# Kernel optimization log

Measured on AMD Instinct MI355X. Metric: run time of the kernel, lower is better.

Reference implementation:

```python
import jax, jax.numpy as jnp
import numpy as np

HEADS = 16
DIM_HEAD = 64
SCALE = DIM_HEAD ** -0.5


def setup_inputs() -> dict:
    key = jax.random.key(0)
    k1, k2, k3, k4 = jax.random.split(key, 4)
    b, n, dim = 2, 2048, 1024
    inner = HEADS * DIM_HEAD  # 1024
    return {
        "x": jax.random.normal(k1, (b, n, dim), dtype=jnp.float32),
        "x1": jax.random.normal(k2, (b, n, dim), dtype=jnp.float32),
        "W_qkv": jax.random.normal(k3, (dim, inner * 3), dtype=jnp.float32) * (dim ** -0.5),
        "W_out": jax.random.normal(k4, (inner, dim), dtype=jnp.float32) * (inner ** -0.5),
        "b_out": jnp.zeros((dim,), dtype=jnp.float32),
    }


def _split_heads(t):
    b, n, hd = t.shape
    return t.reshape(b, n, HEADS, DIM_HEAD).transpose(0, 2, 1, 3)  # b h n d


def _merge_heads(t):
    b, h, n, d = t.shape
    return t.transpose(0, 2, 1, 3).reshape(b, n, h * d)


def reference(x, x1, W_qkv, W_out, b_out):
    qkv = jnp.split(x @ W_qkv, 3, axis=-1)
    qkv1 = jnp.split(x1 @ W_qkv, 3, axis=-1)
    q, k, v = map(_split_heads, qkv)
    q1, k1, v1 = map(_split_heads, qkv1)

    # cross attention: x queries attend to x1 keys/values, and vice versa
    attn = jax.nn.softmax(jnp.einsum('bhnd,bhmd->bhnm', q, k1) * SCALE, axis=-1)
    attn1 = jax.nn.softmax(jnp.einsum('bhnd,bhmd->bhnm', q1, k) * SCALE, axis=-1)
    out = _merge_heads(jnp.einsum('bhnm,bhmd->bhnd', attn, v1))
    out1 = _merge_heads(jnp.einsum('bhnm,bhmd->bhnd', attn1, v))

    out = out @ W_out + b_out
    out1 = out1 @ W_out + b_out
    return out, out1
```

## Files before the change

kernel.cpp:

```cpp
#include <hip/hip_runtime.h>
#include <hip/hip_bf16.h>


typedef __attribute__((ext_vector_type(8))) short short8;
typedef __attribute__((ext_vector_type(4))) float f32x4;
typedef __attribute__((ext_vector_type(16))) float f32x16;

#define MFMA_BF16(a, b, c) __builtin_amdgcn_mfma_f32_16x16x32_bf16((a), (b), (c), 0, 0, 0)
#define MFMA32(a, b, c)    __builtin_amdgcn_mfma_f32_32x32x16_bf16((a), (b), (c), 0, 0, 0)

__device__ __forceinline__ ushort f2bf(float f) {
    __hip_bfloat16 h = __float2bfloat16(f);
    return *reinterpret_cast<ushort*>(&h);
}

__device__ __forceinline__ unsigned pk2(float a, float b) {
    return (unsigned)f2bf(a) | ((unsigned)f2bf(b) << 16);
}

__device__ __forceinline__ void gload_lds16(const void* g, void* l) {
    __builtin_amdgcn_global_load_lds(
        (const __attribute__((address_space(1))) void*)g,
        (__attribute__((address_space(3))) void*)l, 16, 0, 0);
}

__global__ __launch_bounds__(256) void cvt2_k(const float* __restrict__ a,
                                              const float* __restrict__ b,
                                              ushort* __restrict__ out) {
    const int idx = blockIdx.x * 256 + threadIdx.x;
    const int half = 1048576;
    const float* src = (idx < half) ? a : b;
    const int i = (idx < half ? idx : idx - half) * 4;
    float4 v = *(const float4*)(src + i);
    ushort4 o;
    o.x = f2bf(v.x); o.y = f2bf(v.y); o.z = f2bf(v.z); o.w = f2bf(v.w);
    *(ushort4*)(out + (size_t)idx * 4) = o;
}

__global__ __launch_bounds__(256) void transpose_cvt2(const float* __restrict__ wqkv,
                                                      ushort* __restrict__ wqkv_t,
                                                      const float* __restrict__ wout,
                                                      ushort* __restrict__ wout_t) {
    __shared__ ushort tile[32][33];
    int bx = blockIdx.x;
    const float* in; ushort* out; int C;
    if (bx < 96) { in = wqkv; out = wqkv_t; C = 3072; }
    else         { bx -= 96; in = wout; out = wout_t; C = 1024; }
    const int R = 1024;
    const int c0 = bx * 32, r0 = blockIdx.y * 32;
    const int tx = threadIdx.x, ty = threadIdx.y;
#pragma unroll
    for (int i = 0; i < 4; ++i)
        tile[ty * 4 + i][tx] = f2bf(in[(size_t)(r0 + ty * 4 + i) * C + c0 + tx]);
    __syncthreads();
#pragma unroll
    for (int i = 0; i < 4; ++i)
        out[(size_t)(c0 + ty * 4 + i) * R + r0 + tx] = tile[tx][ty * 4 + i];
}

__global__ __launch_bounds__(256) void qkv_gemm(const ushort* __restrict__ xb,
                                                const ushort* __restrict__ wt,
                                                ushort* __restrict__ qb,
                                                ushort* __restrict__ kb,
                                                ushort* __restrict__ vb) {
    __shared__ __align__(16) ushort As[128 * 64];
    __shared__ __align__(16) ushort Bs[128 * 64];

    const int n0 = blockIdx.x * 128;
    const int m0 = blockIdx.y * 128;
    const int t = threadIdx.x;
    const int lane = t & 63, w = t >> 6;
    const int wm = (w >> 1) * 64, wn = (w & 1) * 64;
    const int l16 = lane & 15, lq = lane >> 4;

    const int srow = lane >> 3;
    const int scol = ((lane & 7) * 16) ^ (srow << 4);

    f32x4 acc[4][4] = {};

    for (int k0 = 0; k0 < 1024; k0 += 64) {
        __syncthreads();
#pragma unroll
        for (int c = 0; c < 4; ++c) {
            const int ch = w * 4 + c;
            const int row = ch * 8 + srow;
            gload_lds16((const char*)xb + ((size_t)(m0 + row) * 1024 + k0) * 2 + scol,
                        (char*)As + ch * 1024);
            gload_lds16((const char*)wt + ((size_t)(n0 + row) * 1024 + k0) * 2 + scol,
                        (char*)Bs + ch * 1024);
        }
        __syncthreads();
#pragma unroll
        for (int kc = 0; kc < 2; ++kc) {
            short8 a[4], b[4];
#pragma unroll
            for (int i = 0; i < 4; ++i) {
                const int row = wm + i * 16 + l16;
                a[i] = *(const short8*)((const char*)As + row * 128 +
                                        ((kc * 64 + lq * 16) ^ ((row & 7) << 4)));
            }
#pragma unroll
            for (int j = 0; j < 4; ++j) {
                const int row = wn + j * 16 + l16;
                b[j] = *(const short8*)((const char*)Bs + row * 128 +
                                        ((kc * 64 + lq * 16) ^ ((row & 7) << 4)));
            }
#pragma unroll
            for (int i = 0; i < 4; ++i)
#pragma unroll
                for (int j = 0; j < 4; ++j) acc[i][j] = MFMA_BF16(a[i], b[j], acc[i][j]);
        }
    }

    const int which = (n0 >> 10);
    const float qscale = (which == 0) ? 0.125f : 1.0f;

#pragma unroll
    for (int i = 0; i < 4; ++i) {
#pragma unroll
        for (int jj = 0; jj < 4; ++jj) {
#pragma unroll
            for (int rr = 0; rr < 4; ++rr) {
                const int m = m0 + wm + i * 16 + lq * 4 + rr;
                const int nc = n0 + wn + jj * 16 + l16;
                const ushort bv = f2bf(acc[i][jj][rr] * qscale);
                const int s = m >> 12;
                const int mm = m & 4095;
                const int rem = nc & 1023;
                const int h = rem >> 6, d = rem & 63;
                const int sb = (s << 1) | (mm >> 11);
                const int pos = mm & 2047;
                const size_t bh = (size_t)(sb * 16 + h);
                if (which == 0)      qb[(bh * 2048 + pos) * 64 + d] = bv;
                else if (which == 1) kb[(bh * 2048 + pos) * 64 + d] = bv;
                else                 vb[(bh * 64 + d) * 2048 + pos] = bv;
            }
        }
    }
}

__global__ __launch_bounds__(256, 4) void attn_k(const ushort* __restrict__ qb,
                                                 const ushort* __restrict__ kb,
                                                 const ushort* __restrict__ vb,
                                                 ushort* __restrict__ ob) {
    __shared__ __align__(16) ushort Ks[2][4096];
    __shared__ __align__(16) ushort Vs[2][4096];

    const int t = threadIdx.x, lane = t & 63, w = t >> 6;
    const int l31 = lane & 31, hi = lane >> 5;

    const int lid = blockIdx.x;
    const int xcd = lid & 7, kk = lid >> 3;
    const int qt = kk & 15;
    const int g = xcd + ((kk >> 4) << 3);
    const int h = g & 15, sb = g >> 4;
    const int s = sb >> 1, bb = sb & 1;
    const int kvsb = ((1 - s) << 1) | bb;
    const int q0 = qt * 128 + w * 32;

    const ushort* qp = qb + (size_t)(sb * 16 + h) * 2048 * 64;
    const char* kp = (const char*)(kb + (size_t)(kvsb * 16 + h) * 2048 * 64);
    const char* vp = (const char*)(vb + (size_t)(kvsb * 16 + h) * 64 * 2048);

    short8 qf[4];
#pragma unroll
    for (int c = 0; c < 4; ++c)
        qf[c] = *(const short8*)(qp + (size_t)(q0 + l31) * 64 + c * 16 + hi * 8);

    f32x16 o0 = {}, o1 = {};
    float lsum = 0.f;

    const int swl = ((lane >> 3) & 7) << 4;
    auto stage = [&](int buf, int key0) {
#pragma unroll
        for (int i = 0; i < 2; ++i) {
            const int ch = w * 2 + i;
            const int off = ch * 1024 + lane * 16;
            gload_lds16(kp + (size_t)key0 * 128 + (off ^ swl),
                        (char*)&Ks[buf][0] + ch * 1024);
            const int rd = ch * 8 + (lane >> 3);
            const int cb = (lane & 7) * 16;
            gload_lds16(vp + (size_t)rd * 4096 + (size_t)key0 * 2 + (cb ^ swl),
                        (char*)&Vs[buf][0] + ch * 1024);
        }
    };

    stage(0, 0);
    __syncthreads();

    for (int tt = 0; tt < 32; ++tt) {
        const int cur = tt & 1;
        if (tt < 31) stage(cur ^ 1, (tt + 1) * 64);

        const char* Kc = (const char*)&Ks[cur][0];
        const char* Vc = (const char*)&Vs[cur][0];
        const int sw = (l31 & 7) << 4;

        f32x16 scA = {}, scB = {};
#pragma unroll
        for (int c = 0; c < 4; ++c) {
            const int off = c * 32 + hi * 16;
            short8 ka = *(const short8*)(Kc + l31 * 128 + (off ^ sw));
            short8 kb2 = *(const short8*)(Kc + (32 + l31) * 128 + (off ^ sw));
            scA = MFMA32(ka, qf[c], scA);
            scB = MFMA32(kb2, qf[c], scB);
        }

#pragma unroll
        for (int r = 0; r < 16; ++r) scA[r] = __expf(scA[r]);
#pragma unroll
        for (int r = 0; r < 16; ++r) scB[r] = __expf(scB[r]);
        {
            float sA = (((scA[0] + scA[1]) + (scA[2] + scA[3])) +
                        ((scA[4] + scA[5]) + (scA[6] + scA[7]))) +
                       (((scA[8] + scA[9]) + (scA[10] + scA[11])) +
                        ((scA[12] + scA[13]) + (scA[14] + scA[15])));
            float sB = (((scB[0] + scB[1]) + (scB[2] + scB[3])) +
                        ((scB[4] + scB[5]) + (scB[6] + scB[7]))) +
                       (((scB[8] + scB[9]) + (scB[10] + scB[11])) +
                        ((scB[12] + scB[13]) + (scB[14] + scB[15])));
            lsum += sA + sB;
        }

#define PACK_PV(P, BASE, KS)                                                     \
        {                                                                        \
            unsigned R00 = pk2(P[BASE + 0], P[BASE + 1]);                        \
            unsigned R10 = pk2(P[BASE + 2], P[BASE + 3]);                        \
            unsigned R01 = pk2(P[BASE + 4], P[BASE + 5]);                        \
            unsigned R11 = pk2(P[BASE + 6], P[BASE + 7]);                        \
            unsigned ra = (unsigned)__shfl_xor((int)(hi ? R00 : R01), 32);       \
            unsigned rb = (unsigned)__shfl_xor((int)(hi ? R10 : R11), 32);       \
            union { unsigned u[4]; short8 s8; } ap;                              \
            ap.u[0] = hi ? ra : R00;                                             \
            ap.u[1] = hi ? rb : R10;                                             \
            ap.u[2] = hi ? R01 : ra;                                             \
            ap.u[3] = hi ? R11 : rb;                                             \
            const int vo = (KS) * 32 + hi * 16;                                  \
            short8 v0 = *(const short8*)(Vc + l31 * 128 + (vo ^ sw));            \
            short8 v1 = *(const short8*)(Vc + (32 + l31) * 128 + (vo ^ sw));     \
            o0 = MFMA32(ap.s8, v0, o0);                                          \
            o1 = MFMA32(ap.s8, v1, o1);                                          \
        }
        PACK_PV(scA, 0, 0)
        PACK_PV(scA, 8, 1)
        PACK_PV(scB, 0, 2)
        PACK_PV(scB, 8, 3)
#undef PACK_PV

        __syncthreads();
    }

    const float lf = lsum + __shfl_xor(lsum, 32);
    const size_t obase = (size_t)(sb * 2048 + q0) * 1024 + h * 64 + l31;
#pragma unroll
    for (int r = 0; r < 16; ++r) {
        const int qrow = (r & 3) + 8 * (r >> 2) + 4 * hi;
        const float invl = 1.f / __shfl(lf, qrow);
        ob[obase + (size_t)qrow * 1024]      = f2bf(o0[r] * invl);
        ob[obase + (size_t)qrow * 1024 + 32] = f2bf(o1[r] * invl);
    }
}

__global__ __launch_bounds__(256) void out_gemm(const ushort* __restrict__ ob,
                                                const ushort* __restrict__ wot,
                                                const float* __restrict__ bias,
                                                float* __restrict__ out) {
    __shared__ __align__(16) ushort As[128 * 64];
    __shared__ __align__(16) ushort Bs[128 * 64];

    const int n0 = blockIdx.x * 128;
    const int m0 = blockIdx.y * 128;
    const int t = threadIdx.x;
    const int lane = t & 63, w = t >> 6;
    const int wm = (w >> 1) * 64, wn = (w & 1) * 64;
    const int l16 = lane & 15, lq = lane >> 4;

    const int srow = lane >> 3;
    const int scol = ((lane & 7) * 16) ^ (srow << 4);

    f32x4 acc[4][4] = {};

    for (int k0 = 0; k0 < 1024; k0 += 64) {
        __syncthreads();
#pragma unroll
        for (int c = 0; c < 4; ++c) {
            const int ch = w * 4 + c;
            const int row = ch * 8 + srow;
            gload_lds16((const char*)ob + ((size_t)(m0 + row) * 1024 + k0) * 2 + scol,
                        (char*)As + ch * 1024);
            gload_lds16((const char*)wot + ((size_t)(n0 + row) * 1024 + k0) * 2 + scol,
                        (char*)Bs + ch * 1024);
        }
        __syncthreads();
#pragma unroll
        for (int kc = 0; kc < 2; ++kc) {
            short8 a[4], b[4];
#pragma unroll
            for (int i = 0; i < 4; ++i) {
                const int row = wm + i * 16 + l16;
                a[i] = *(const short8*)((const char*)As + row * 128 +
                                        ((kc * 64 + lq * 16) ^ ((row & 7) << 4)));
            }
#pragma unroll
            for (int j = 0; j < 4; ++j) {
                const int row = wn + j * 16 + l16;
                b[j] = *(const short8*)((const char*)Bs + row * 128 +
                                        ((kc * 64 + lq * 16) ^ ((row & 7) << 4)));
            }
#pragma unroll
            for (int i = 0; i < 4; ++i)
#pragma unroll
                for (int j = 0; j < 4; ++j) acc[i][j] = MFMA_BF16(a[i], b[j], acc[i][j]);
        }
    }

    float biasf[4];
#pragma unroll
    for (int jj = 0; jj < 4; ++jj) biasf[jj] = bias[n0 + wn + jj * 16 + l16];

#pragma unroll
    for (int i = 0; i < 4; ++i)
#pragma unroll
        for (int jj = 0; jj < 4; ++jj)
#pragma unroll
            for (int rr = 0; rr < 4; ++rr) {
                const int m = m0 + wm + i * 16 + lq * 4 + rr;
                const int nc = n0 + wn + jj * 16 + l16;
                out[(size_t)m * 1024 + nc] = acc[i][jj][rr] + biasf[jj];
            }
}

extern "C" void kernel_launch(void* const* d_in, const int* in_sizes, int n_in,
                              void* d_out, int out_size, void* d_ws, size_t ws_size,
                              hipStream_t stream) {
    (void)out_size; (void)ws_size;
    const float *x = nullptr, *x1 = nullptr, *wqkv = nullptr, *wout = nullptr, *bias = nullptr;
    for (int i = 0; i < n_in; ++i) {
        const int sz = in_sizes[i];
        const float* p = (const float*)d_in[i];
        if (sz == 4194304)      { if (!x) x = p; else x1 = p; }
        else if (sz == 3145728) wqkv = p;
        else if (sz == 1048576) wout = p;
        else if (sz == 1024)    bias = p;
    }
    float* out = (float*)d_out;

    ushort* ws      = (ushort*)d_ws;
    ushort* wqkv_t  = ws;
    ushort* wout_t  = wqkv_t + 3072 * 1024;
    ushort* xb      = wout_t + 1024 * 1024;
    ushort* qbuf    = xb + 8388608;
    ushort* kbuf    = qbuf + 8388608;
    ushort* vbuf    = kbuf + 8388608;
    ushort* obuf    = xb;

    cvt2_k<<<8192, 256, 0, stream>>>(x, x1, xb);
    transpose_cvt2<<<dim3(128, 32), dim3(32, 8), 0, stream>>>(wqkv, wqkv_t, wout, wout_t);
    qkv_gemm<<<dim3(24, 64), 256, 0, stream>>>(xb, wqkv_t, qbuf, kbuf, vbuf);
    attn_k<<<1024, 256, 0, stream>>>(qbuf, kbuf, vbuf, obuf);
    out_gemm<<<dim3(8, 64), 256, 0, stream>>>(obuf, wout_t, bias, out);
}
```

Baseline: 307.3 us.

## Fuse prep kernels, use exp2 with folded log2e, MFMA row sums, packed bf16 cvt

Merges the input-conversion and weight-transpose kernels into a single launch, saving one kernel launch. Folds log2(e) into the Q scale so attention can use exp2 instead of exp. The softmax denominator is now computed with an extra MFMA against a ones vector instead of scalar adds and a final shuffle. Probability packing uses the hardware v_cvt_pk_bf16_f32 instruction, and s_setprio hints are added around the MFMA sections. The MFMA row sum is taken from bf16-rounded probabilities, which changes normalization numerics slightly, and it adds MFMA work to each tile.

```diff
diff --git a/kernel.cpp b/kernel.cpp
--- a/kernel.cpp
+++ b/kernel.cpp
@@ -14,8 +14,10 @@
     return *reinterpret_cast<ushort*>(&h);
 }
 
-__device__ __forceinline__ unsigned pk2(float a, float b) {
-    return (unsigned)f2bf(a) | ((unsigned)f2bf(b) << 16);
+__device__ __forceinline__ unsigned cvtpk(float lo, float hi) {
+    unsigned r;
+    asm("v_cvt_pk_bf16_f32 %0, %1, %2" : "=v"(r) : "v"(lo), "v"(hi));
+    return r;
 }
 
 __device__ __forceinline__ void gload_lds16(const void* g, void* l) {
@@ -24,31 +26,35 @@
         (__attribute__((address_space(3))) void*)l, 16, 0, 0);
 }
 
-__global__ __launch_bounds__(256) void cvt2_k(const float* __restrict__ a,
-                                              const float* __restrict__ b,
-                                              ushort* __restrict__ out) {
-    const int idx = blockIdx.x * 256 + threadIdx.x;
-    const int half = 1048576;
-    const float* src = (idx < half) ? a : b;
-    const int i = (idx < half ? idx : idx - half) * 4;
-    float4 v = *(const float4*)(src + i);
-    ushort4 o;
-    o.x = f2bf(v.x); o.y = f2bf(v.y); o.z = f2bf(v.z); o.w = f2bf(v.w);
-    *(ushort4*)(out + (size_t)idx * 4) = o;
-}
-
-__global__ __launch_bounds__(256) void transpose_cvt2(const float* __restrict__ wqkv,
-                                                      ushort* __restrict__ wqkv_t,
-                                                      const float* __restrict__ wout,
-                                                      ushort* __restrict__ wout_t) {
+__global__ __launch_bounds__(256) void prep_k(const float* __restrict__ x,
+                                              const float* __restrict__ x1,
+                                              ushort* __restrict__ xb,
+                                              const float* __restrict__ wqkv,
+                                              ushort* __restrict__ wqkv_t,
+                                              const float* __restrict__ wout,
+                                              ushort* __restrict__ wout_t) {
     __shared__ ushort tile[32][33];
-    int bx = blockIdx.x;
+    const int b = blockIdx.x;
+    if (b < 8192) {
+        const int idx = b * 256 + threadIdx.x;
+        const int half = 1048576;
+        const float* src = (idx < half) ? x : x1;
+        const int i = (idx < half ? idx : idx - half) * 4;
+        float4 v = *(const float4*)(src + i);
+        ushort4 o;
+        o.x = f2bf(v.x); o.y = f2bf(v.y); o.z = f2bf(v.z); o.w = f2bf(v.w);
+        *(ushort4*)(xb + (size_t)idx * 4) = o;
+        return;
+    }
+    const int id = b - 8192;
+    int bx = id & 127;
+    const int by = id >> 7;
     const float* in; ushort* out; int C;
     if (bx < 96) { in = wqkv; out = wqkv_t; C = 3072; }
     else         { bx -= 96; in = wout; out = wout_t; C = 1024; }
     const int R = 1024;
-    const int c0 = bx * 32, r0 = blockIdx.y * 32;
-    const int tx = threadIdx.x, ty = threadIdx.y;
+    const int c0 = bx * 32, r0 = by * 32;
+    const int tx = threadIdx.x & 31, ty = threadIdx.x >> 5;
 #pragma unroll
     for (int i = 0; i < 4; ++i)
         tile[ty * 4 + i][tx] = f2bf(in[(size_t)(r0 + ty * 4 + i) * C + c0 + tx]);
@@ -113,7 +119,7 @@
     }
 
     const int which = (n0 >> 10);
-    const float qscale = (which == 0) ? 0.125f : 1.0f;
+    const float qscale = (which == 0) ? 0.18033688f : 1.0f;
 
 #pragma unroll
     for (int i = 0; i < 4; ++i) {
@@ -167,8 +173,12 @@
     for (int c = 0; c < 4; ++c)
         qf[c] = *(const short8*)(qp + (size_t)(q0 + l31) * 64 + c * 16 + hi * 8);
 
+    short8 ones;
+#pragma unroll
+    for (int j = 0; j < 8; ++j) ones[j] = (short)0x3F80;
+
     f32x16 o0 = {}, o1 = {};
-    float lsum = 0.f;
+    f32x16 l_acc = {};
 
     const int swl = ((lane >> 3) & 7) << 4;
     auto stage = [&](int buf, int key0) {
@@ -197,6 +207,7 @@
         const int sw = (l31 & 7) << 4;
 
         f32x16 scA = {}, scB = {};
+        __builtin_amdgcn_s_setprio(1);
 #pragma unroll
         for (int c = 0; c < 4; ++c) {
             const int off = c * 32 + hi * 16;
@@ -205,29 +216,20 @@
             scA = MFMA32(ka, qf[c], scA);
             scB = MFMA32(kb2, qf[c], scB);
         }
-
-#pragma unroll
-        for (int r = 0; r < 16; ++r) scA[r] = __expf(scA[r]);
-#pragma unroll
-        for (int r = 0; r < 16; ++r) scB[r] = __expf(scB[r]);
-        {
-            float sA = (((scA[0] + scA[1]) + (scA[2] + scA[3])) +
-                        ((scA[4] + scA[5]) + (scA[6] + scA[7]))) +
-                       (((scA[8] + scA[9]) + (scA[10] + scA[11])) +
-                        ((scA[12] + scA[13]) + (scA[14] + scA[15])));
-            float sB = (((scB[0] + scB[1]) + (scB[2] + scB[3])) +
-                        ((scB[4] + scB[5]) + (scB[6] + scB[7]))) +
-                       (((scB[8] + scB[9]) + (scB[10] + scB[11])) +
-                        ((scB[12] + scB[13]) + (scB[14] + scB[15])));
-            lsum += sA + sB;
-        }
-
+        __builtin_amdgcn_s_setprio(0);
+
+#pragma unroll
+        for (int r = 0; r < 16; ++r) scA[r] = __builtin_exp2f(scA[r]);
+#pragma unroll
+        for (int r = 0; r < 16; ++r) scB[r] = __builtin_exp2f(scB[r]);
+
+        __builtin_amdgcn_s_setprio(1);
 #define PACK_PV(P, BASE, KS)                                                     \
         {                                                                        \
-            unsigned R00 = pk2(P[BASE + 0], P[BASE + 1]);                        \
-            unsigned R10 = pk2(P[BASE + 2], P[BASE + 3]);                        \
-            unsigned R01 = pk2(P[BASE + 4], P[BASE + 5]);                        \
-            unsigned R11 = pk2(P[BASE + 6], P[BASE + 7]);                        \
+            unsigned R00 = cvtpk(P[BASE + 0], P[BASE + 1]);                      \
+            unsigned R10 = cvtpk(P[BASE + 2], P[BASE + 3]);                      \
+            unsigned R01 = cvtpk(P[BASE + 4], P[BASE + 5]);                      \
+            unsigned R11 = cvtpk(P[BASE + 6], P[BASE + 7]);                      \
             unsigned ra = (unsigned)__shfl_xor((int)(hi ? R00 : R01), 32);       \
             unsigned rb = (unsigned)__shfl_xor((int)(hi ? R10 : R11), 32);       \
             union { unsigned u[4]; short8 s8; } ap;                              \
@@ -240,22 +242,23 @@
             short8 v1 = *(const short8*)(Vc + (32 + l31) * 128 + (vo ^ sw));     \
             o0 = MFMA32(ap.s8, v0, o0);                                          \
             o1 = MFMA32(ap.s8, v1, o1);                                          \
+            l_acc = MFMA32(ap.s8, ones, l_acc);                                  \
         }
         PACK_PV(scA, 0, 0)
         PACK_PV(scA, 8, 1)
         PACK_PV(scB, 0, 2)
         PACK_PV(scB, 8, 3)
 #undef PACK_PV
-
-        __syncthreads();
-    }
-
-    const float lf = lsum + __shfl_xor(lsum, 32);
+        __builtin_amdgcn_s_setprio(0);
+
+        __syncthreads();
+    }
+
     const size_t obase = (size_t)(sb * 2048 + q0) * 1024 + h * 64 + l31;
 #pragma unroll
     for (int r = 0; r < 16; ++r) {
         const int qrow = (r & 3) + 8 * (r >> 2) + 4 * hi;
-        const float invl = 1.f / __shfl(lf, qrow);
+        const float invl = 1.f / l_acc[r];
         ob[obase + (size_t)qrow * 1024]      = f2bf(o0[r] * invl);
         ob[obase + (size_t)qrow * 1024 + 32] = f2bf(o1[r] * invl);
     }
@@ -354,8 +357,7 @@
     ushort* vbuf    = kbuf + 8388608;
     ushort* obuf    = xb;
 
-    cvt2_k<<<8192, 256, 0, stream>>>(x, x1, xb);
-    transpose_cvt2<<<dim3(128, 32), dim3(32, 8), 0, stream>>>(wqkv, wqkv_t, wout, wout_t);
+    prep_k<<<12288, 256, 0, stream>>>(x, x1, xb, wqkv, wqkv_t, wout, wout_t);
     qkv_gemm<<<dim3(24, 64), 256, 0, stream>>>(xb, wqkv_t, qbuf, kbuf, vbuf);
     attn_k<<<1024, 256, 0, stream>>>(qbuf, kbuf, vbuf, obuf);
     out_gemm<<<dim3(8, 64), 256, 0, stream>>>(obuf, wout_t, bias, out);
```

New measurement: 343.7 us. 1.12x slower.
